# Performance work log

Hardware: AMD Instinct MI355X
Metric: run time of the kernel (lower is better)

## Reference

```python
import jax, jax.numpy as jnp
import numpy as np
import math

B, S, DIM = 2, 2048, 2048
NH = 16
HD = DIM // NH  # 128
RANK = 32


def setup_inputs() -> dict:
    key = jax.random.key(0)
    ks = jax.random.split(key, 10)
    x = jax.random.normal(ks[0], (B, S, DIM), dtype=jnp.float32)
    # causal additive mask (use -1e9 instead of -inf for grad-safety)
    mask = jnp.where(jnp.tril(jnp.ones((S, S), dtype=bool)), 0.0, -1e9).astype(jnp.float32)[None, None]
    # rotary frequencies, as in llama: theta = 10000^{-2i/d}
    inv_freq = 1.0 / (10000.0 ** (jnp.arange(0, HD, 2, dtype=jnp.float32) / HD))  # [HD/2]
    t = jnp.arange(S, dtype=jnp.float32)
    freqs = jnp.outer(t, inv_freq)  # [S, HD/2]
    freqs_cos = jnp.cos(freqs)
    freqs_sin = jnp.sin(freqs)
    scale = 0.02
    wq = jax.random.normal(ks[1], (DIM, DIM), dtype=jnp.float32) * scale
    wk = jax.random.normal(ks[2], (DIM, DIM), dtype=jnp.float32) * scale
    wv = jax.random.normal(ks[3], (DIM, DIM), dtype=jnp.float32) * scale
    wo = jax.random.normal(ks[4], (DIM, DIM), dtype=jnp.float32) * scale
    wa_q = jax.random.normal(ks[5], (RANK, DIM), dtype=jnp.float32) * 0.02
    wa_k = jax.random.normal(ks[6], (RANK, DIM), dtype=jnp.float32) * 0.02
    return {"x": x, "mask": mask, "freqs_cos": freqs_cos, "freqs_sin": freqs_sin,
            "wq": wq, "wk": wk, "wv": wv, "wo": wo, "wa_q": wa_q, "wa_k": wa_k}


def _apply_rope(t, cos, sin):
    # t: [B, S, H, HD]; cos/sin: [S, HD/2]
    tr = t.reshape(*t.shape[:-1], HD // 2, 2)
    tre, tim = tr[..., 0], tr[..., 1]
    c = cos[None, :, None, :]
    s = sin[None, :, None, :]
    out_re = tre * c - tim * s
    out_im = tre * s + tim * c
    return jnp.stack([out_re, out_im], axis=-1).reshape(t.shape)


def reference(x, mask, freqs_cos, freqs_sin, wq, wk, wv, wo, wa_q, wa_k):
    bsz, seqlen, dim = x.shape
    xq = (x @ wq.T).reshape(bsz, seqlen, NH, HD)
    xk = (x @ wk.T).reshape(bsz, seqlen, NH, HD)
    xv = (x @ wv.T).reshape(bsz, seqlen, NH, HD)
    # low-rank adaptive gate (computed on detached x in the original)
    xd = jax.lax.stop_gradient(x)
    xq_h = xd @ wa_q.T  # [B, S, 32]
    xk_h = xd @ wa_k.T  # [B, S, 32]
    adaptive_mask = jnp.einsum('bqr,bkr->bqk', xq_h, xk_h)  # [B, S, S]

    xq = _apply_rope(xq, freqs_cos, freqs_sin)
    xk = _apply_rope(xk, freqs_cos, freqs_sin)

    q = xq.transpose(0, 2, 1, 3)  # [B, H, S, HD]
    k = xk.transpose(0, 2, 1, 3)
    v = xv.transpose(0, 2, 1, 3)

    scores = jnp.einsum('bhqd,bhkd->bhqk', q, k) / math.sqrt(HD)
    scores = scores + mask
    scores = jax.nn.softmax(scores.astype(jnp.float32), axis=-1).astype(q.dtype)
    scores = scores * jax.nn.sigmoid(adaptive_mask)[:, None]  # gate, broadcast over heads
    out = jnp.einsum('bhqk,bhkd->bhqd', scores, v)
    out = out.transpose(0, 2, 1, 3).reshape(bsz, seqlen, -1)
    return out @ wo.T
```

## Files before the change

### kernel.cpp

```cpp
#include <hip/hip_runtime.h>

typedef __attribute__((ext_vector_type(8))) short short8v;
typedef __attribute__((ext_vector_type(4))) short short4v;
typedef __attribute__((ext_vector_type(4))) float floatx4;

#define S_    2048
#define DIM_  2048
#define NW_   6400
#define VOFF_ 4352

#define ASG(p) ((__attribute__((address_space(1))) void*)(p))
#define ASL(p) ((__attribute__((address_space(3))) void*)(p))

__device__ __forceinline__ short f2bf(float f){
  union { float f; unsigned u; } c; c.f = f;
  unsigned u = c.u;
  unsigned r = (u + 0x7fffu + ((u >> 16) & 1u)) >> 16;
  return (short)r;
}
__device__ __forceinline__ float bf2f(short s){
  union { unsigned u; float f; } c; c.u = ((unsigned)(unsigned short)s) << 16;
  return c.f;
}

__global__ __launch_bounds__(256) void cvt_k(const float* __restrict__ in,
                                             short* __restrict__ out, int n){
  int i = blockIdx.x*256 + threadIdx.x;
  int idx = i*4;
  if (idx >= n) return;
  floatx4 v = *(const floatx4*)(in + idx);
  short4v o;
  o[0]=f2bf(v[0]); o[1]=f2bf(v[1]); o[2]=f2bf(v[2]); o[3]=f2bf(v[3]);
  *(short4v*)(out + idx) = o;
}

__global__ __launch_bounds__(256)
void cvt_w(const float* wq, const float* waq, const float* wak,
           const float* wk, const float* wv, const float* wo,
           short* Wcat, short* wob){
  const float* src; short* dst; int n;
  switch (blockIdx.y){
    case 0: src=wq;  dst=Wcat;                 n=4194304; break;
    case 1: src=waq; dst=Wcat+(size_t)2048*2048; n=65536; break;
    case 2: src=wak; dst=Wcat+(size_t)2080*2048; n=65536; break;
    case 3: src=wk;  dst=Wcat+(size_t)2112*2048; n=4194304; break;
    case 4: src=wv;  dst=Wcat+(size_t)4352*2048; n=4194304; break;
    case 5: src=wo;  dst=wob;                  n=4194304; break;
    default: {
      int idx = (blockIdx.x*256 + threadIdx.x)*4;
      if (idx < 393216){
        short4v z = {0,0,0,0};
        *(short4v*)(Wcat + (size_t)4160*2048 + idx) = z;
      }
      return;
    }
  }
  int idx = (blockIdx.x*256 + threadIdx.x)*4;
  if (idx >= n) return;
  floatx4 v = *(const floatx4*)(src + idx);
  short4v o;
  o[0]=f2bf(v[0]); o[1]=f2bf(v[1]); o[2]=f2bf(v[2]); o[3]=f2bf(v[3]);
  *(short4v*)(dst + idx) = o;
}

__global__ __launch_bounds__(512,2)
void gemm_qkv(const short* __restrict__ A, const short* __restrict__ B,
              short* __restrict__ Cout, short* __restrict__ Vt){
  __shared__ short SH[65536];
  const int K = 2048;
  int tid = threadIdx.x;
  int wave = tid>>6, lane = tid&63, quad = lane>>4, l16 = lane&15;
  int wm_i = wave>>2, wn_i = wave&3;

  int bid = blockIdx.x;
  int swz = (bid&7)*50 + (bid>>3);
  int m0 = (swz & 15)*256;
  int n0 = (swz >> 4)*256;

  int srow = tid>>2;
  int sseg = (tid&3) ^ ((srow ^ (srow>>2)) & 3);
  const short* aS = A + (size_t)(m0 + srow)*K + sseg*8;
  const short* bS = B + (size_t)(n0 + srow)*K + sseg*8;
  int sdst = wave*512;

  int sx   = (l16 ^ (l16>>2)) & 3;
  int aoff = (wm_i*128 + l16)*32 + (quad^sx)*8;
  int boff = (wn_i*64  + l16)*32 + (quad^sx)*8;

  floatx4 acc[8][4] = {};
  short8v afA[8], afB[8], bfA[4], bfB[4];

#define QSTAGE(src, chunk) do{ \
    __builtin_amdgcn_global_load_lds(ASG(src), ASL(&SH[(chunk)+sdst]), 16, 0, 0); \
    __builtin_amdgcn_global_load_lds(ASG((src) + (size_t)128*2048), ASL(&SH[(chunk)+sdst+4096]), 16, 0, 0); \
  }while(0)
#define QBAR  asm volatile("s_barrier" ::: "memory")
#define QW4   asm volatile("s_waitcnt vmcnt(4)" ::: "memory")
#define MFMA_ __builtin_amdgcn_mfma_f32_16x16x32_bf16

  QSTAGE(aS,            0);
  QSTAGE(bS,        32768);
  QSTAGE(aS+32,      8192);
  QSTAGE(bS+32, 32768+8192);
  QW4;
  QBAR;
  #pragma unroll
  for (int mf=0; mf<4; ++mf) afA[mf] = *(short8v*)&SH[0     + mf*512 + aoff];
  #pragma unroll
  for (int nf=0; nf<4; ++nf) bfA[nf] = *(short8v*)&SH[32768 + nf*512 + boff];
  QSTAGE(aS + 64, 16384);

  for (int t=0; t<32; ++t){
    int buf = t&1, nb = buf^1;
    int A0c = buf*16384,        A1c = A0c+8192;
    int B0c = 32768+buf*16384,  B1c = B0c+8192;
    int A0n = nb*16384,         A1n = A0n+8192;
    int B0n = 32768+nb*16384,   B1n = B0n+8192;
    int kn  = ((t+1)&31)*64;
    int kn2 = ((t+2)&31)*64;

    #pragma unroll
    for (int mf=4; mf<8; ++mf) afA[mf] = *(short8v*)&SH[A0c + mf*512 + aoff];
    QSTAGE(bS + kn, B0n);
    QW4;
    QBAR;
    __builtin_amdgcn_s_setprio(1);
    #pragma unroll
    for (int mf=0; mf<4; ++mf)
      #pragma unroll
      for (int nf=0; nf<4; ++nf)
        acc[mf][nf] = MFMA_(afA[mf], bfA[nf], acc[mf][nf], 0,0,0);
    __builtin_amdgcn_s_setprio(0);

    #pragma unroll
    for (int mf=0; mf<4; ++mf) afB[mf] = *(short8v*)&SH[A1c + mf*512 + aoff];
    #pragma unroll
    for (int nf=0; nf<4; ++nf) bfB[nf] = *(short8v*)&SH[B1c + nf*512 + boff];
    QSTAGE(aS + kn + 32, A1n);
    QBAR;
    __builtin_amdgcn_s_setprio(1);
    #pragma unroll
    for (int mf=4; mf<8; ++mf)
      #pragma unroll
      for (int nf=0; nf<4; ++nf)
        acc[mf][nf] = MFMA_(afA[mf], bfA[nf], acc[mf][nf], 0,0,0);
    __builtin_amdgcn_s_setprio(0);

    #pragma unroll
    for (int mf=4; mf<8; ++mf) afB[mf] = *(short8v*)&SH[A1c + mf*512 + aoff];
    QSTAGE(bS + kn + 32, B1n);
    QW4;
    QBAR;
    __builtin_amdgcn_s_setprio(1);
    #pragma unroll
    for (int mf=0; mf<4; ++mf)
      #pragma unroll
      for (int nf=0; nf<4; ++nf)
        acc[mf][nf] = MFMA_(afB[mf], bfB[nf], acc[mf][nf], 0,0,0);
    __builtin_amdgcn_s_setprio(0);

    #pragma unroll
    for (int mf=0; mf<4; ++mf) afA[mf] = *(short8v*)&SH[A0n + mf*512 + aoff];
    #pragma unroll
    for (int nf=0; nf<4; ++nf) bfA[nf] = *(short8v*)&SH[B0n + nf*512 + boff];
    QSTAGE(aS + kn2, A0c);
    QBAR;
    __builtin_amdgcn_s_setprio(1);
    #pragma unroll
    for (int mf=4; mf<8; ++mf)
      #pragma unroll
      for (int nf=0; nf<4; ++nf)
        acc[mf][nf] = MFMA_(afB[mf], bfB[nf], acc[mf][nf], 0,0,0);
    __builtin_amdgcn_s_setprio(0);
  }

  __syncthreads();

  if (n0 < VOFF_){
    #pragma unroll
    for (int mf=0; mf<8; ++mf)
      #pragma unroll
      for (int r=0; r<4; ++r){
        size_t gm = (size_t)(m0 + wm_i*128 + mf*16 + quad*4 + r);
        #pragma unroll
        for (int nf=0; nf<4; ++nf)
          Cout[gm*NW_ + n0 + wn_i*64 + nf*16 + l16] = f2bf(acc[mf][nf][r]);
      }
  } else {
    short* T = SH;
    #pragma unroll
    for (int mf=0; mf<8; ++mf){
      int mb = wm_i*128 + mf*16 + quad*4;
      int mc = mb>>3, mi = mb&7;
      #pragma unroll
      for (int nf=0; nf<4; ++nf){
        int n = wn_i*64 + nf*16 + l16;
        short4v p;
        p[0]=f2bf(acc[mf][nf][0]); p[1]=f2bf(acc[mf][nf][1]);
        p[2]=f2bf(acc[mf][nf][2]); p[3]=f2bf(acc[mf][nf][3]);
        *(short4v*)&T[n*256 + ((mc ^ (n&31))*8) + mi] = p;
      }
    }
    __syncthreads();
    int f = tid>>1, half = tid&1;
    size_t vbase = (size_t)(n0 - VOFF_ + f)*4096 + m0;
    #pragma unroll
    for (int c=0; c<16; ++c){
      int cc = half*16 + c;
      short8v v = *(short8v*)&T[f*256 + ((cc ^ (f&31))*8)];
      *(short8v*)&Vt[vbase + cc*8] = v;
    }
  }
#undef QSTAGE
#undef QBAR
#undef QW4
#undef MFMA_
}

__global__ __launch_bounds__(256,4)
void gemm_nt_f32(const short* __restrict__ A, const short* __restrict__ B,
                 float* __restrict__ Cout, int M, int N, int K){
  __shared__ short As[128][64];
  __shared__ short Bs[128][64];
  int tid = threadIdx.x;
  int wave = tid>>6, lane = tid&63, quad = lane>>4, l16 = lane&15;
  int l7 = l16&7;
  int m0 = blockIdx.x*128, n0 = blockIdx.y*128;
  int wm = (wave>>1)*64, wn = (wave&1)*64;
  floatx4 acc[4][4] = {};

  int lr = lane>>3;
  int sw = (lane&7) ^ lr;
  const short* Abase = A + (size_t)(m0 + wave*32 + lr)*K + sw*8;
  const short* Bbase = B + (size_t)(n0 + wave*32 + lr)*K + sw*8;

  for (int k0 = 0; k0 < K; k0 += 64){
    __syncthreads();
    #pragma unroll
    for (int i=0;i<4;i++){
      __builtin_amdgcn_global_load_lds(ASG(Abase + (size_t)(i*8)*K + k0),
                                       ASL(&As[wave*32 + i*8][0]), 16, 0, 0);
      __builtin_amdgcn_global_load_lds(ASG(Bbase + (size_t)(i*8)*K + k0),
                                       ASL(&Bs[wave*32 + i*8][0]), 16, 0, 0);
    }
    __syncthreads();
    #pragma unroll
    for (int ks=0; ks<2; ks++){
      short8v af[4], bf[4];
      #pragma unroll
      for (int i=0;i<4;i++) af[i] = *(short8v*)&As[wm + i*16 + l16][((ks*4+quad)^l7)*8];
      #pragma unroll
      for (int j=0;j<4;j++) bf[j] = *(short8v*)&Bs[wn + j*16 + l16][((ks*4+quad)^l7)*8];
      #pragma unroll
      for (int i=0;i<4;i++)
        #pragma unroll
        for (int j=0;j<4;j++)
          acc[i][j] = __builtin_amdgcn_mfma_f32_16x16x32_bf16(af[i], bf[j], acc[i][j], 0,0,0);
    }
  }
  #pragma unroll
  for (int i=0;i<4;i++)
    #pragma unroll
    for (int r=0;r<4;r++){
      int gm = m0 + wm + i*16 + quad*4 + r;
      #pragma unroll
      for (int j=0;j<4;j++){
        int gn = n0 + wn + j*16 + l16;
        Cout[(size_t)gm*N + gn] = acc[i][j][r];
      }
    }
}

__global__ __launch_bounds__(256) void rope_k(short* __restrict__ X,
                                              const float* __restrict__ fcos,
                                              const float* __restrict__ fsin){
  int i = blockIdx.x*256 + threadIdx.x;
  int row = i >> 10;
  int p = i & 1023;
  int s = row & (S_-1);
  int pp = p & 63;
  float c = fcos[s*64+pp], sn = fsin[s*64+pp];
  size_t a = (size_t)row*NW_ + 2112 + p*2;
  int v = *(int*)(X + a);
  float re = bf2f((short)(v & 0xffff)), im = bf2f((short)(v >> 16));
  float orr = re*c - im*sn, oi = re*sn + im*c;
  *(int*)(X + a) = ((int)(unsigned short)f2bf(oi) << 16) | (unsigned short)f2bf(orr);
}

__global__ __launch_bounds__(256)
void gate_k(const short* __restrict__ X, short* __restrict__ G){
  int kt = blockIdx.x, qt = blockIdx.y, b = blockIdx.z;
  if (kt > qt) return;
  int tid = threadIdx.x, wave = tid>>6, lane = tid&63, quad = lane>>4, l16 = lane&15;
  const float NL2E = -1.44269504f;

  short8v qh = *(const short8v*)&X[(size_t)(b*2048 + qt*64 + wave*16 + l16)*NW_ + 2048 + quad*8];
  floatx4 am[4];
  #pragma unroll
  for (int j=0;j<4;j++){
    short8v kh = *(const short8v*)&X[(size_t)(b*2048 + kt*64 + j*16 + l16)*NW_ + 2080 + quad*8];
    floatx4 z = {0.f,0.f,0.f,0.f};
    am[j] = __builtin_amdgcn_mfma_f32_16x16x32_bf16(qh, kh, z, 0,0,0);
  }
  short* Gd = G + (((size_t)(b*32 + kt)*2048) + qt*64 + wave*16 + quad*4)*64 + l16*4;
  #pragma unroll
  for (int r=0;r<4;r++){
    short4v sv;
    #pragma unroll
    for (int j=0;j<4;j++){
      float g = __builtin_amdgcn_rcpf(1.f + __builtin_amdgcn_exp2f(am[j][r]*NL2E));
      sv[j] = f2bf(g);
    }
    *(short4v*)(Gd + (size_t)r*64) = sv;
  }
}

__global__ __launch_bounds__(256,2)
void flash_k(const short* __restrict__ Qc, const short* __restrict__ Vt,
             const short* __restrict__ G, const float* __restrict__ fcos,
             const float* __restrict__ fsin, short* __restrict__ O){
  int h = blockIdx.x, pi = blockIdx.y, b = blockIdx.z;
  int tid = threadIdx.x, wave = tid>>6, lane = tid&63, quad = lane>>4, l16 = lane&15;
  int l7 = l16&7;

  __shared__ short Ks [64][128];
  __shared__ short Vts[128][64];
  __shared__ short Ps [4][16][72];

  const float CS = 1.44269504f * 0.08838834764831845f;

  for (int ph = 0; ph < 2; ph++){
    int qt = ph ? pi : 31 - pi;
    int srow = qt*64 + wave*16 + l16;
    size_t qrow = (size_t)(b*2048 + srow);
    short8v qf[4];
    #pragma unroll
    for (int ks=0;ks<4;ks++)
      qf[ks] = *(const short8v*)&Qc[qrow*NW_ + h*128 + ks*32 + quad*8];
    #pragma unroll
    for (int ks=0;ks<4;ks++)
      #pragma unroll
      for (int jj=0;jj<4;jj++){
        float re = bf2f(qf[ks][2*jj]), im = bf2f(qf[ks][2*jj+1]);
        int p = ks*16 + quad*4 + jj;
        float c = fcos[srow*64 + p], sn = fsin[srow*64 + p];
        qf[ks][2*jj]   = f2bf(re*c - im*sn);
        qf[ks][2*jj+1] = f2bf(re*sn + im*c);
      }

    floatx4 oacc[8] = {};
    float lp[4] = {0.f,0.f,0.f,0.f};

    for (int kt=0; kt<=qt; kt++){
      int k0 = kt*64;
      __syncthreads();
      {
        const short* Ksrc = Qc + ((size_t)(b*2048 + k0 + wave*16))*NW_ + 2112 + h*128;
        int r4 = lane>>4, c16 = lane&15;
        #pragma unroll
        for (int j=0;j<4;j++)
          __builtin_amdgcn_global_load_lds(
            ASG(Ksrc + (size_t)(j*4 + r4)*NW_ + ((c16 ^ r4 ^ ((j&1)*4))*8)),
            ASL(&Ks[wave*16 + j*4][0]), 16, 0, 0);
        const short* Vsrc = Vt + ((size_t)(h*128 + wave*32 + (lane>>3)))*4096 + b*2048 + k0
                            + (((lane&7) ^ (lane>>3))*8);
        #pragma unroll
        for (int j=0;j<4;j++)
          __builtin_amdgcn_global_load_lds(
            ASG(Vsrc + (size_t)(j*8)*4096),
            ASL(&Vts[wave*32 + j*8][0]), 16, 0, 0);
      }
      __syncthreads();

      const short* gb = G + (((size_t)(b*32 + kt)*2048) + qt*64 + wave*16 + quad*4)*64 + l16*4;
      short4v g4[4];
      #pragma unroll
      for (int r=0;r<4;r++) g4[r] = *(const short4v*)(gb + (size_t)r*64);

      floatx4 sacc[4] = {};
      #pragma unroll
      for (int j=0;j<4;j++)
        #pragma unroll
        for (int ks2=0;ks2<4;ks2++){
          short8v kf = *(short8v*)&Ks[j*16+l16][((ks2*4+quad)^l7)*8];
          sacc[j] = __builtin_amdgcn_mfma_f32_16x16x32_bf16(qf[ks2], kf, sacc[j], 0,0,0);
        }

      bool diag = (kt == qt);
      int qbase = wave*16 + quad*4;
      #pragma unroll
      for (int j=0;j<4;j++){
        int kin = j*16 + l16;
        #pragma unroll
        for (int r=0;r<4;r++){
          bool keep = !diag || (kin <= qbase + r);
          float p = keep ? __builtin_amdgcn_exp2f(sacc[j][r]*CS) : 0.f;
          lp[r] += p;
          Ps[wave][quad*4+r][j*16+l16] = f2bf(p * bf2f(g4[r][j]));
        }
      }

      #pragma unroll
      for (int ks2=0; ks2<2; ks2++){
        short8v pf = *(short8v*)&Ps[wave][l16][ks2*32 + quad*8];
        #pragma unroll
        for (int dt=0; dt<8; dt++){
          short8v vf = *(short8v*)&Vts[dt*16 + l16][((ks2*4+quad)^l7)*8];
          oacc[dt] = __builtin_amdgcn_mfma_f32_16x16x32_bf16(pf, vf, oacc[dt], 0,0,0);
        }
      }
    }

    #pragma unroll
    for (int r=0;r<4;r++)
      #pragma unroll
      for (int off=1; off<16; off<<=1)
        lp[r] += __shfl_xor(lp[r], off, 64);
    #pragma unroll
    for (int r=0;r<4;r++){
      float inv = __builtin_amdgcn_rcpf(lp[r]);
      size_t orow = (size_t)(b*2048 + qt*64 + wave*16 + quad*4 + r);
      #pragma unroll
      for (int dt=0;dt<8;dt++)
        O[orow*2048 + h*128 + dt*16 + l16] = f2bf(oacc[dt][r]*inv);
    }
  }
}

extern "C" void kernel_launch(void* const* d_in, const int* in_sizes, int n_in,
                              void* d_out, int out_size, void* d_ws, size_t ws_size,
                              hipStream_t stream){
  const float* x    = (const float*)d_in[0];
  const float* fcos = (const float*)d_in[2];
  const float* fsin = (const float*)d_in[3];
  const float* wq   = (const float*)d_in[4];
  const float* wk   = (const float*)d_in[5];
  const float* wv   = (const float*)d_in[6];
  const float* wo   = (const float*)d_in[7];
  const float* waq  = (const float*)d_in[8];
  const float* wak  = (const float*)d_in[9];
  float* out = (float*)d_out;

  char* ws = (char*)d_ws;
  size_t off = 0;
  short* xb   = (short*)(ws + off); off += (size_t)4096*2048*2;
  short* Wcat = (short*)(ws + off); off += (size_t)NW_*2048*2;
  short* wob  = (short*)(ws + off); off += (size_t)2048*2048*2;
  short* XQKV = (short*)(ws + off); off += (size_t)4096*NW_*2;
  short* Vtb  = (short*)(ws + off); off += (size_t)2048*4096*2;
  short* G    = xb;
  short* Ob   = Wcat;

  cvt_k<<<8192,256,0,stream>>>(x, xb, 8388608);
  cvt_w<<<dim3(4096,7),256,0,stream>>>(wq, waq, wak, wk, wv, wo, Wcat, wob);

  gemm_qkv<<<dim3(400),512,0,stream>>>(xb, Wcat, XQKV, Vtb);

  rope_k<<<16384,256,0,stream>>>(XQKV, fcos, fsin);
  gate_k<<<dim3(32,32,2),256,0,stream>>>(XQKV, G);

  flash_k<<<dim3(16,16,2),256,0,stream>>>(XQKV, Vtb, G, fcos, fsin, Ob);

  gemm_nt_f32<<<dim3(32,16),256,0,stream>>>(Ob, wob, out, 4096, 2048, 2048);
}
```

Before: 399.8 us.

## Double-buffer K/V tiles in flash kernel to overlap loads with MFMA

The flash attention kernel now keeps two LDS buffers for the K and V tiles. It issues the async global-to-LDS loads for the next key tile before running the current tile's QK and PV MFMAs, and replaces the two __syncthreads per iteration with a single vmcnt wait plus barrier. The goal is to hide global memory latency behind compute. LDS use rises from about 41KB to about 74KB per block, which may limit the two-blocks-per-CU occupancy target. The raw vmcnt(0) wait also drains the gate loads.

```diff
diff --git a/kernel.cpp b/kernel.cpp
--- a/kernel.cpp
+++ b/kernel.cpp
@@ -323,11 +323,28 @@
   int tid = threadIdx.x, wave = tid>>6, lane = tid&63, quad = lane>>4, l16 = lane&15;
   int l7 = l16&7;
 
-  __shared__ short Ks [64][128];
-  __shared__ short Vts[128][64];
+  __shared__ short Ks [2][64][128];
+  __shared__ short Vts[2][128][64];
   __shared__ short Ps [4][16][72];
 
   const float CS = 1.44269504f * 0.08838834764831845f;
+  int r4 = lane>>4, c16 = lane&15;
+
+#define FSTAGE(kt_, bb) do{ \
+    const short* Ksrc = Qc + ((size_t)(b*2048 + (kt_)*64 + wave*16))*NW_ + 2112 + h*128; \
+    _Pragma("unroll") \
+    for (int j=0;j<4;j++) \
+      __builtin_amdgcn_global_load_lds( \
+        ASG(Ksrc + (size_t)(j*4 + r4)*NW_ + ((c16 ^ r4 ^ ((j&1)*4))*8)), \
+        ASL(&Ks[bb][wave*16 + j*4][0]), 16, 0, 0); \
+    const short* Vsrc = Vt + ((size_t)(h*128 + wave*32 + (lane>>3)))*4096 + b*2048 + (kt_)*64 \
+                        + (((lane&7) ^ (lane>>3))*8); \
+    _Pragma("unroll") \
+    for (int j=0;j<4;j++) \
+      __builtin_amdgcn_global_load_lds( \
+        ASG(Vsrc + (size_t)(j*8)*4096), \
+        ASL(&Vts[bb][wave*32 + j*8][0]), 16, 0, 0); \
+  }while(0)
 
   for (int ph = 0; ph < 2; ph++){
     int qt = ph ? pi : 31 - pi;
@@ -351,38 +368,27 @@
     floatx4 oacc[8] = {};
     float lp[4] = {0.f,0.f,0.f,0.f};
 
+    __builtin_amdgcn_s_barrier();
+    FSTAGE(0, 0);
+
     for (int kt=0; kt<=qt; kt++){
-      int k0 = kt*64;
-      __syncthreads();
-      {
-        const short* Ksrc = Qc + ((size_t)(b*2048 + k0 + wave*16))*NW_ + 2112 + h*128;
-        int r4 = lane>>4, c16 = lane&15;
-        #pragma unroll
-        for (int j=0;j<4;j++)
-          __builtin_amdgcn_global_load_lds(
-            ASG(Ksrc + (size_t)(j*4 + r4)*NW_ + ((c16 ^ r4 ^ ((j&1)*4))*8)),
-            ASL(&Ks[wave*16 + j*4][0]), 16, 0, 0);
-        const short* Vsrc = Vt + ((size_t)(h*128 + wave*32 + (lane>>3)))*4096 + b*2048 + k0
-                            + (((lane&7) ^ (lane>>3))*8);
-        #pragma unroll
-        for (int j=0;j<4;j++)
-          __builtin_amdgcn_global_load_lds(
-            ASG(Vsrc + (size_t)(j*8)*4096),
-            ASL(&Vts[wave*32 + j*8][0]), 16, 0, 0);
-      }
-      __syncthreads();
+      int buf = kt&1;
+      asm volatile("s_waitcnt vmcnt(0)" ::: "memory");
+      __builtin_amdgcn_s_barrier();
 
       const short* gb = G + (((size_t)(b*32 + kt)*2048) + qt*64 + wave*16 + quad*4)*64 + l16*4;
       short4v g4[4];
       #pragma unroll
       for (int r=0;r<4;r++) g4[r] = *(const short4v*)(gb + (size_t)r*64);
+
+      if (kt < qt) FSTAGE(kt+1, buf^1);
 
       floatx4 sacc[4] = {};
       #pragma unroll
       for (int j=0;j<4;j++)
         #pragma unroll
         for (int ks2=0;ks2<4;ks2++){
-          short8v kf = *(short8v*)&Ks[j*16+l16][((ks2*4+quad)^l7)*8];
+          short8v kf = *(short8v*)&Ks[buf][j*16+l16][((ks2*4+quad)^l7)*8];
           sacc[j] = __builtin_amdgcn_mfma_f32_16x16x32_bf16(qf[ks2], kf, sacc[j], 0,0,0);
         }
 
@@ -405,7 +411,7 @@
         short8v pf = *(short8v*)&Ps[wave][l16][ks2*32 + quad*8];
         #pragma unroll
         for (int dt=0; dt<8; dt++){
-          short8v vf = *(short8v*)&Vts[dt*16 + l16][((ks2*4+quad)^l7)*8];
+          short8v vf = *(short8v*)&Vts[buf][dt*16 + l16][((ks2*4+quad)^l7)*8];
           oacc[dt] = __builtin_amdgcn_mfma_f32_16x16x32_bf16(pf, vf, oacc[dt], 0,0,0);
         }
       }
@@ -425,6 +431,7 @@
         O[orow*2048 + h*128 + dt*16 + l16] = f2bf(oacc[dt][r]*inv);
     }
   }
+#undef FSTAGE
 }
 
 extern "C" void kernel_launch(void* const* d_in, const int* in_sizes, int n_in,
```

After: 403.6 us. Within noise of the previous version (+1.0%).
